# Kernel optimization log

Measured on AMD Instinct MI355X. Metric: run time of the kernel, lower is better.

## Reference

```python
import jax, jax.numpy as jnp
import numpy as np

TAU = 1.0
LOSS_WEIGHT = 1.0
N = 4_000_000


def setup_inputs() -> dict:
    key = jax.random.key(0)
    k1, k2 = jax.random.split(key)

    def make_boxes(k):
        u = jax.random.uniform(k, (N, 5), dtype=jnp.float32)
        xy = u[:, :2] * 1024.0                 # centers in a 1024px image
        wh = u[:, 2:4] * 100.0 + 4.0           # box sizes in [4, 104)
        r = (u[:, 4:5] - 0.5) * jnp.pi         # angle in [-pi/2, pi/2)
        return jnp.concatenate([xy, wh, r], axis=-1)

    return {"pred": make_boxes(k1), "target": make_boxes(k2)}


def xy_wh_r_2_xy_sigma(xywhr):
    """(N,5) rbox -> (mu (N,2), sigma (N,2,2)) via R @ (S/2)^2 @ R^T closed form."""
    xy = xywhr[..., :2]
    wh = jnp.clip(xywhr[..., 2:4], 1e-7, 1e7)
    r = xywhr[..., 4]
    c, s = jnp.cos(r), jnp.sin(r)
    a = (0.5 * wh[..., 0]) ** 2  # (w/2)^2
    b = (0.5 * wh[..., 1]) ** 2  # (h/2)^2
    s00 = a * c * c + b * s * s
    s11 = a * s * s + b * c * c
    s01 = (a - b) * s * c
    sigma = jnp.stack(
        [jnp.stack([s00, s01], -1), jnp.stack([s01, s11], -1)], -2
    )  # (N,2,2)
    return xy, sigma


def _det2(m):
    return m[..., 0, 0] * m[..., 1, 1] - m[..., 0, 1] * m[..., 1, 0]


def _inv2(m):
    det = _det2(m)
    adj = jnp.stack(
        [jnp.stack([m[..., 1, 1], -m[..., 0, 1]], -1),
         jnp.stack([-m[..., 1, 0], m[..., 0, 0]], -1)], -2)
    return adj / det[..., None, None]


def kld_loss(mu_p, sigma_p, mu_t, sigma_t, tau):
    delta = mu_p - mu_t                                # (N,2)
    sigma_t_inv = _inv2(sigma_t)                       # (N,2,2)
    # delta^T Sigma_t^{-1} delta
    term1 = jnp.einsum('ni,nij,nj->n', delta, sigma_t_inv, delta)
    # tr(Sigma_t^{-1} Sigma_p) + log(det Sigma_t / det Sigma_p)
    tr = jnp.einsum('nij,nji->n', sigma_t_inv, sigma_p)
    term2 = tr + jnp.log(_det2(sigma_t) / _det2(sigma_p))
    dis = term1 + term2 - 2.0
    kl_dis = jnp.maximum(dis, 1e-6)
    # fun == 'log1p'
    loss = 1.0 - 1.0 / (tau + jnp.log1p(kl_dis))
    return loss[:, None]                               # (N,1) like torch version


def reference(pred, target):
    mu_p, sigma_p = xy_wh_r_2_xy_sigma(pred)
    mu_t, sigma_t = xy_wh_r_2_xy_sigma(target)
    return kld_loss(mu_p, sigma_p, mu_t, sigma_t, TAU) * LOSS_WEIGHT
```

## Files before the change

### kernel.cpp

```cpp
#include <hip/hip_runtime.h>
#include <math.h>
#include <stdint.h>

#ifndef TAU_CONST
#define TAU_CONST 1.0f
#endif


__device__ __forceinline__ void rbox_to_gauss(float x, float y, float w, float h, float r,
                                              float& mx, float& my,
                                              float& s00, float& s01, float& s11, float& det) {
    w = fminf(fmaxf(w, 1e-7f), 1e7f);
    h = fminf(fmaxf(h, 1e-7f), 1e7f);
    float a = 0.25f * w * w;
    float b = 0.25f * h * h;
    float s2, c2;
    __sincosf(r + r, &s2, &c2);
    float hs = 0.5f * (a + b);
    float hd = 0.5f * (a - b);
    s00 = fmaf(hd, c2, hs);
    s11 = fmaf(-hd, c2, hs);
    s01 = hd * s2;
    det = a * b;
    mx = x; my = y;
}

__device__ __forceinline__ float kld_row(const float* p, const float* t) {
    float pmx, pmy, p00, p01, p11, dp;
    float tmx, tmy, t00, t01, t11, dt;
    rbox_to_gauss(p[0], p[1], p[2], p[3], p[4], pmx, pmy, p00, p01, p11, dp);
    rbox_to_gauss(t[0], t[1], t[2], t[3], t[4], tmx, tmy, t00, t01, t11, dt);
    float dx = pmx - tmx, dy = pmy - tmy;
    float inv_dt = __builtin_amdgcn_rcpf(dt);
    float inv_dp = __builtin_amdgcn_rcpf(dp);
    float term1 = (dx * dx * t11 - 2.0f * dx * dy * t01 + dy * dy * t00) * inv_dt;
    float tr = (t11 * p00 + t00 * p11 - 2.0f * t01 * p01) * inv_dt;
    float term2 = tr + __logf(dt * inv_dp);
    float dis = term1 + term2 - 2.0f;
    float kl = fmaxf(dis, 1e-6f);
    float l1p = __logf(1.0f + kl);
    return 1.0f - __builtin_amdgcn_rcpf(TAU_CONST + l1p);
}


__device__ __forceinline__ void gload_lds16(const void* g, void* l) {
    __builtin_amdgcn_global_load_lds((const __attribute__((address_space(1))) uint32_t*)g,
                                     (__attribute__((address_space(3))) uint32_t*)l,
                                     16, 0, 0);
}

#define ROWS_PER_TILE 256
#define FLOATS_PER_TILE (ROWS_PER_TILE * 5)

__global__ void __launch_bounds__(256, 8)
gdloss_pipe_kernel(const float* __restrict__ pred,
                   const float* __restrict__ target,
                   float* __restrict__ out, int ntiles) {
    __shared__ float lds[2][2 * FLOATS_PER_TILE];
    const int tid = threadIdx.x;
    const int wv  = tid >> 6;
    const int ln  = tid & 63;
    const int stride = gridDim.x;

    int t = blockIdx.x;
    if (t < ntiles) {
        for (int c = wv; c < 10; c += 4) {
            const float* g = (c < 5)
                ? (pred   + (long long)t * FLOATS_PER_TILE + c * 256 + ln * 4)
                : (target + (long long)t * FLOATS_PER_TILE + (c - 5) * 256 + ln * 4);
            gload_lds16(g, &lds[0][c * 256]);
        }
    }

    int buf = 0;
    for (; t < ntiles; t += stride) {
        __syncthreads();
        int tn = t + stride;
        if (tn < ntiles) {
            for (int c = wv; c < 10; c += 4) {
                const float* g = (c < 5)
                    ? (pred   + (long long)tn * FLOATS_PER_TILE + c * 256 + ln * 4)
                    : (target + (long long)tn * FLOATS_PER_TILE + (c - 5) * 256 + ln * 4);
                gload_lds16(g, &lds[buf ^ 1][c * 256]);
            }
        }
        const float* lp = &lds[buf][5 * tid];
        const float* lt = &lds[buf][FLOATS_PER_TILE + 5 * tid];
        float p[5], tt[5];
#pragma unroll
        for (int k = 0; k < 5; ++k) { p[k] = lp[k]; tt[k] = lt[k]; }
        out[(long long)t * ROWS_PER_TILE + tid] = kld_row(p, tt);
        buf ^= 1;
    }
}

__global__ void gdloss_tail_kernel(const float* __restrict__ pred,
                                   const float* __restrict__ target,
                                   float* __restrict__ out, int start, int n) {
    int i = start + blockIdx.x * blockDim.x + threadIdx.x;
    if (i >= n) return;
    float p[5], t[5];
#pragma unroll
    for (int k = 0; k < 5; ++k) {
        p[k] = pred[5 * i + k];
        t[k] = target[5 * i + k];
    }
    out[i] = kld_row(p, t);
}

extern "C" void kernel_launch(void* const* d_in, const int* in_sizes, int n_in,
                              void* d_out, int out_size, void* d_ws, size_t ws_size,
                              hipStream_t stream) {
    const float* pred   = (const float*)d_in[0];
    const float* target = (const float*)d_in[1];
    float* out = (float*)d_out;
    int n      = in_sizes[0] / 5;
    int ntiles = n / ROWS_PER_TILE;
    if (ntiles > 0) {
        int blocks = ntiles < 2048 ? ntiles : 2048;
        gdloss_pipe_kernel<<<blocks, 256, 0, stream>>>(pred, target, out, ntiles);
    }
    int start = ntiles * ROWS_PER_TILE;
    int rem = n - start;
    if (rem > 0) {
        int tb = (rem + 255) / 256;
        gdloss_tail_kernel<<<tb, 256, 0, stream>>>(pred, target, out, start, n);
    }
}
```

Before: 180.4 us.

## Prefetch tiles into registers with nontemporal vector loads and store 4 rows per thread

Replaces the async global-to-LDS double-buffered pipeline with a register-staged prefetch. Each thread issues 16-byte nontemporal loads of the next 1024-row tile into registers, writes the current tile to a single LDS buffer, and computes four rows per thread with one vectorized nontemporal store. This aims to widen memory transactions and raise bytes in flight per thread. In exchange it adds a second barrier per iteration, needs more registers (launch bounds lowered to 4), and uses half the grid size.

```diff
diff --git a/kernel.cpp b/kernel.cpp
--- a/kernel.cpp
+++ b/kernel.cpp
@@ -5,6 +5,8 @@
 #ifndef TAU_CONST
 #define TAU_CONST 1.0f
 #endif
+
+typedef float v4f __attribute__((ext_vector_type(4)));
 
 
 __device__ __forceinline__ void rbox_to_gauss(float x, float y, float w, float h, float r,
@@ -43,54 +45,64 @@
 }
 
 
-__device__ __forceinline__ void gload_lds16(const void* g, void* l) {
-    __builtin_amdgcn_global_load_lds((const __attribute__((address_space(1))) uint32_t*)g,
-                                     (__attribute__((address_space(3))) uint32_t*)l,
-                                     16, 0, 0);
-}
+#define TILE_ROWS 1024
+#define TILE_FLOATS (TILE_ROWS * 5)
 
-#define ROWS_PER_TILE 256
-#define FLOATS_PER_TILE (ROWS_PER_TILE * 5)
-
-__global__ void __launch_bounds__(256, 8)
-gdloss_pipe_kernel(const float* __restrict__ pred,
-                   const float* __restrict__ target,
-                   float* __restrict__ out, int ntiles) {
-    __shared__ float lds[2][2 * FLOATS_PER_TILE];
+__global__ void __launch_bounds__(256, 4)
+gdloss_regpipe_kernel(const float* __restrict__ pred,
+                      const float* __restrict__ target,
+                      float* __restrict__ out, int ntiles) {
+    __shared__ float lds[2 * TILE_FLOATS];
     const int tid = threadIdx.x;
-    const int wv  = tid >> 6;
-    const int ln  = tid & 63;
     const int stride = gridDim.x;
 
+    v4f pv[5], tv[5];
     int t = blockIdx.x;
     if (t < ntiles) {
-        for (int c = wv; c < 10; c += 4) {
-            const float* g = (c < 5)
-                ? (pred   + (long long)t * FLOATS_PER_TILE + c * 256 + ln * 4)
-                : (target + (long long)t * FLOATS_PER_TILE + (c - 5) * 256 + ln * 4);
-            gload_lds16(g, &lds[0][c * 256]);
+        const v4f* pb = (const v4f*)(pred   + (long long)t * TILE_FLOATS);
+        const v4f* tb = (const v4f*)(target + (long long)t * TILE_FLOATS);
+#pragma unroll
+        for (int k = 0; k < 5; ++k) {
+            pv[k] = __builtin_nontemporal_load(pb + k * 256 + tid);
+            tv[k] = __builtin_nontemporal_load(tb + k * 256 + tid);
         }
     }
 
-    int buf = 0;
     for (; t < ntiles; t += stride) {
         __syncthreads();
+#pragma unroll
+        for (int k = 0; k < 5; ++k) {
+            ((v4f*)lds)[k * 256 + tid] = pv[k];
+            ((v4f*)(lds + TILE_FLOATS))[k * 256 + tid] = tv[k];
+        }
+        __syncthreads();
+
         int tn = t + stride;
         if (tn < ntiles) {
-            for (int c = wv; c < 10; c += 4) {
-                const float* g = (c < 5)
-                    ? (pred   + (long long)tn * FLOATS_PER_TILE + c * 256 + ln * 4)
-                    : (target + (long long)tn * FLOATS_PER_TILE + (c - 5) * 256 + ln * 4);
-                gload_lds16(g, &lds[buf ^ 1][c * 256]);
+            const v4f* pb = (const v4f*)(pred   + (long long)tn * TILE_FLOATS);
+            const v4f* tb = (const v4f*)(target + (long long)tn * TILE_FLOATS);
+#pragma unroll
+            for (int k = 0; k < 5; ++k) {
+                pv[k] = __builtin_nontemporal_load(pb + k * 256 + tid);
+                tv[k] = __builtin_nontemporal_load(tb + k * 256 + tid);
             }
         }
-        const float* lp = &lds[buf][5 * tid];
-        const float* lt = &lds[buf][FLOATS_PER_TILE + 5 * tid];
-        float p[5], tt[5];
+
+        const v4f* lp = (const v4f*)&lds[20 * tid];
+        const v4f* lt = (const v4f*)&lds[TILE_FLOATS + 20 * tid];
+        float pf[20], tf[20];
 #pragma unroll
-        for (int k = 0; k < 5; ++k) { p[k] = lp[k]; tt[k] = lt[k]; }
-        out[(long long)t * ROWS_PER_TILE + tid] = kld_row(p, tt);
-        buf ^= 1;
+        for (int k = 0; k < 5; ++k) {
+            v4f a = lp[k], b = lt[k];
+            pf[4 * k + 0] = a.x; pf[4 * k + 1] = a.y; pf[4 * k + 2] = a.z; pf[4 * k + 3] = a.w;
+            tf[4 * k + 0] = b.x; tf[4 * k + 1] = b.y; tf[4 * k + 2] = b.z; tf[4 * k + 3] = b.w;
+        }
+        v4f o;
+        o.x = kld_row(pf + 0,  tf + 0);
+        o.y = kld_row(pf + 5,  tf + 5);
+        o.z = kld_row(pf + 10, tf + 10);
+        o.w = kld_row(pf + 15, tf + 15);
+        __builtin_nontemporal_store(o, (v4f*)out + (long long)t * 256 + tid);
     }
 }
 
@@ -115,12 +127,12 @@
     const float* target = (const float*)d_in[1];
     float* out = (float*)d_out;
     int n      = in_sizes[0] / 5;
-    int ntiles = n / ROWS_PER_TILE;
+    int ntiles = n / TILE_ROWS;
     if (ntiles > 0) {
-        int blocks = ntiles < 2048 ? ntiles : 2048;
-        gdloss_pipe_kernel<<<blocks, 256, 0, stream>>>(pred, target, out, ntiles);
+        int blocks = ntiles < 1024 ? ntiles : 1024;
+        gdloss_regpipe_kernel<<<blocks, 256, 0, stream>>>(pred, target, out, ntiles);
     }
-    int start = ntiles * ROWS_PER_TILE;
+    int start = ntiles * TILE_ROWS;
     int rem = n - start;
     if (rem > 0) {
         int tb = (rem + 255) / 256;
```

New measurement: 169.9 us. -5.8%, faster.
